# Optimization experiments

Hardware: AMD Instinct MI355X
Metric: run time of the kernel (lower is better)

The kernel has to match this reference:

```python
import jax, jax.numpy as jnp
import numpy as np

WORD_TOTAL = 1_000_000
POS_TOTAL = 123
DIM = 50        # word embedding dim
DWPE = 5        # position embedding dim
C = 230         # conv filters (dimensionC)
WIN = 3         # conv window
REL = 53        # relationTotal
B = 1024        # bag size (number of sentences)
L = 128         # sentence length


def setup_inputs() -> dict:
    key = jax.random.key(0)
    ks = jax.random.split(key, 12)
    con = np.sqrt(6.0 / (C + REL))
    con1 = np.sqrt(6.0 / ((DWPE + DIM) * WIN))
    inp = {
        "sen": jax.random.randint(ks[0], (B, L), 0, WORD_TOTAL),
        "p1": jax.random.randint(ks[1], (B, L), 0, POS_TOTAL),
        "p2": jax.random.randint(ks[2], (B, L), 0, POS_TOTAL),
        "wordVec": jax.random.normal(ks[3], (WORD_TOTAL, DIM), jnp.float32) * 0.05,
        "posVec1": jax.random.normal(ks[4], (POS_TOTAL, DWPE), jnp.float32) * con1,
        "posVec2": jax.random.normal(ks[5], (POS_TOTAL, DWPE), jnp.float32) * con1,
        "Wv": jax.random.normal(ks[6], (WIN, DIM, C), jnp.float32) * 0.05,
        "Wp1": jax.random.normal(ks[7], (WIN, DWPE, C), jnp.float32) * 0.05,
        "Wp2": jax.random.normal(ks[8], (WIN, DWPE, C), jnp.float32) * 0.05,
        "bv": jnp.zeros((C,), jnp.float32),
        "bp1": jnp.zeros((C,), jnp.float32),
        "bp2": jnp.zeros((C,), jnp.float32),
        "attW": jax.random.normal(ks[9], (C, C), jnp.float32) * con,
        "MR": jax.random.normal(ks[10], (C, REL), jnp.float32) * 0.05,
        "MRb": jnp.zeros((REL,), jnp.float32),
        "rel": 7,
    }
    return inp


def _conv_full_width(emb, W):
    Lout = emb.shape[1] - WIN + 1
    wins = jnp.stack([emb[:, j:j + Lout, :] for j in range(WIN)], axis=0)
    return jnp.einsum('jbld,jdc->blc', wins, W)  # [B, Lout, C]


def reference(sen, p1, p2, wordVec, posVec1, posVec2, Wv, bv, Wp1, bp1, Wp2, bp2, attW, MR, MRb, rel):
    # ---- encode: per-sentence PCNN-style encoder, batched over the bag ----
    ev = wordVec[sen]   # [B, L, DIM]
    e1 = posVec1[p1]    # [B, L, DWPE]
    e2 = posVec2[p2]    # [B, L, DWPE]
    c = (_conv_full_width(ev, Wv) + bv
         + _conv_full_width(e1, Wp1) + bp1
         + _conv_full_width(e2, Wp2) + bp2)          # [B, Lout, C]
    cnn_output = jnp.tanh(jnp.max(c, axis=1))          # [B, C]
    # ---- selective attention over the bag (training=False: dropout identity) ----
    scores = (cnn_output @ attW) @ MR + MRb            # [B, REL]
    weight = jax.nn.softmax(scores[:, rel])            # [B] = exp/sum(exp)
    att_output = jnp.sum(weight[:, None] * cnn_output, axis=0)[None, :]  # [1, C]
    output = jax.nn.softmax(att_output @ MR + MRb)     # [1, REL]
    return (output, att_output, cnn_output, weight[:, None])
```

## Files before the change

kernel.cpp:

```cpp
#include <hip/hip_runtime.h>
#include <math.h>

#define CCH 230
#define REL 53
#define BAG 1024
#define SLEN 128
#define LOUT 126

typedef __bf16 bf16x8 __attribute__((ext_vector_type(8)));
typedef float f32x4 __attribute__((ext_vector_type(4)));

#define WS_BF_USHORTS (16 * 6 * 64 * 8)
#define WS_BSUM 24576
#define WS_V    24832
#define WS_SCORES 25088

__device__ __forceinline__ unsigned short f2bf(float f) {
    unsigned u = __builtin_bit_cast(unsigned, f);
    unsigned r = (u + 0x7fffu + ((u >> 16) & 1u)) >> 16;
    return (unsigned short)r;
}

__global__ void pa_kernel(const float* __restrict__ Wv, const float* __restrict__ Wp1,
                          const float* __restrict__ Wp2, const float* __restrict__ bv,
                          const float* __restrict__ bp1, const float* __restrict__ bp2,
                          const float* __restrict__ attW, const float* __restrict__ MR,
                          const int* __restrict__ relp, float* __restrict__ ws) {
    if (blockIdx.x < 193) {
        int idx = blockIdx.x * 256 + threadIdx.x;
        if (idx < WS_BF_USHORTS) {
            int j = idx & 7;
            int lane = (idx >> 3) & 63;
            int q = idx >> 9;
            int ks = q % 6, ntile = q / 6;
            int n = ntile * 16 + (lane & 15);
            int k = ks * 32 + (lane >> 4) * 8 + j;
            float v = 0.f;
            if (k < 180 && n < CCH) {
                int jw = k / 60;
                int d = k - jw * 60;
                if (d < 50)      v = Wv[(jw * 50 + d) * CCH + n];
                else if (d < 55) v = Wp1[(jw * 5 + (d - 50)) * CCH + n];
                else             v = Wp2[(jw * 5 + (d - 55)) * CCH + n];
            }
            ((unsigned short*)ws)[idx] = f2bf(v);
        } else {
            int ch = idx - WS_BF_USHORTS;
            float v = 0.f;
            if (ch < CCH) v = bv[ch] + bp1[ch] + bp2[ch];
            ws[WS_BSUM + ch] = v;
        }
    } else {
        int i = (blockIdx.x - 193) * 4 + (threadIdx.x >> 6);
        int lane = threadIdx.x & 63;
        if (i < CCH) {
            int rel = *relp;
            float s = 0.f;
            for (int j = lane; j < CCH; j += 64) s += attW[i * CCH + j] * MR[j * REL + rel];
            for (int off = 32; off > 0; off >>= 1) s += __shfl_down(s, off, 64);
            if (lane == 0) ws[WS_V + i] = s;
        }
    }
}

__global__ __launch_bounds__(512, 4) void conv_kernel(
    const int* __restrict__ sen, const int* __restrict__ p1, const int* __restrict__ p2,
    const float* __restrict__ wordVec, const float* __restrict__ posVec1,
    const float* __restrict__ posVec2, const float* __restrict__ ws,
    const float* __restrict__ MRb, const int* __restrict__ relp,
    float* __restrict__ cnn_out, float* __restrict__ scores) {
    __shared__ __align__(16) unsigned short x_lds[132 * 60];
    __shared__ int s_idx[3][SLEN];
    __shared__ float s_red[8];
    const int b = blockIdx.x;
    const int tid = threadIdx.x;
    const int lane = tid & 63, w = tid >> 6;
    const int quad = lane >> 4, l16 = lane & 15;
    const unsigned short* wsu = (const unsigned short*)ws;

    bf16x8 bfrag[6][2];
    #pragma unroll
    for (int ks = 0; ks < 6; ++ks)
        #pragma unroll
        for (int nt = 0; nt < 2; ++nt) {
            int ntile = w * 2 + nt;
            bfrag[ks][nt] = *reinterpret_cast<const bf16x8*>(wsu + ((ntile * 6 + ks) * 64 + lane) * 8);
        }

    if (tid < 384) {
        int a = tid >> 7, i = tid & 127;
        const int* src = (a == 0) ? sen : (a == 1) ? p1 : p2;
        s_idx[a][i] = src[b * SLEN + i];
    }
    __syncthreads();

    {
        int l = tid >> 2, t = tid & 3;
        if (t < 3) {
            float v[16];
            const float* base = wordVec + s_idx[0][l] * 50 + t * 16;
            #pragma unroll
            for (int k2 = 0; k2 < 8; ++k2) {
                float2 f = *reinterpret_cast<const float2*>(base + 2 * k2);
                v[2 * k2] = f.x; v[2 * k2 + 1] = f.y;
            }
            ushort4* dst = reinterpret_cast<ushort4*>(x_lds + l * 60 + t * 16);
            #pragma unroll
            for (int q = 0; q < 4; ++q) {
                ushort4 o;
                o.x = f2bf(v[4 * q + 0]); o.y = f2bf(v[4 * q + 1]);
                o.z = f2bf(v[4 * q + 2]); o.w = f2bf(v[4 * q + 3]);
                dst[q] = o;
            }
        } else {
            float v[12];
            float2 wv = *reinterpret_cast<const float2*>(wordVec + s_idx[0][l] * 50 + 48);
            v[0] = wv.x; v[1] = wv.y;
            int i1 = s_idx[1][l] * 5, i2 = s_idx[2][l] * 5;
            #pragma unroll
            for (int j = 0; j < 5; ++j) { v[2 + j] = posVec1[i1 + j]; v[7 + j] = posVec2[i2 + j]; }
            ushort4* dst = reinterpret_cast<ushort4*>(x_lds + l * 60 + 48);
            #pragma unroll
            for (int q = 0; q < 3; ++q) {
                ushort4 o;
                o.x = f2bf(v[4 * q + 0]); o.y = f2bf(v[4 * q + 1]);
                o.z = f2bf(v[4 * q + 2]); o.w = f2bf(v[4 * q + 3]);
                dst[q] = o;
            }
        }
    }
    if (tid < 16) {
        int l = SLEN + (tid >> 2), t = tid & 3;
        ushort4 z; z.x = z.y = z.z = z.w = 0;
        ushort4* dst = reinterpret_cast<ushort4*>(x_lds + l * 60 + ((t < 3) ? t * 16 : 48));
        if (t < 3) { dst[0] = z; dst[1] = z; dst[2] = z; dst[3] = z; }
        else       { dst[0] = z; dst[1] = z; dst[2] = z; }
    }
    __syncthreads();

    f32x4 acc[8][2];
    #pragma unroll
    for (int mt = 0; mt < 8; ++mt)
        #pragma unroll
        for (int nt = 0; nt < 2; ++nt) acc[mt][nt] = (f32x4){0.f, 0.f, 0.f, 0.f};

    union AU { uint2 u2[2]; bf16x8 v; };

    #pragma unroll
    for (int ks = 0; ks < 6; ++ks) {
        int kg = ks * 4 + quad;
        #pragma unroll
        for (int mt = 0; mt < 8; ++mt) {
            int m = mt * 16 + l16;
            const uint2* ap = reinterpret_cast<const uint2*>(x_lds + m * 60 + kg * 8);
            AU a; a.u2[0] = ap[0]; a.u2[1] = ap[1];
            #pragma unroll
            for (int nt = 0; nt < 2; ++nt)
                acc[mt][nt] = __builtin_amdgcn_mfma_f32_16x16x32_bf16(a.v, bfrag[ks][nt], acc[mt][nt], 0, 0, 0);
        }
    }

    float vals[2];
    #pragma unroll
    for (int nt = 0; nt < 2; ++nt) {
        float mv = -3.0e38f;
        #pragma unroll
        for (int mt = 0; mt < 8; ++mt) {
            #pragma unroll
            for (int r = 0; r < 4; ++r) {
                int l = mt * 16 + quad * 4 + r;
                if (l < LOUT) mv = fmaxf(mv, acc[mt][nt][r]);
            }
        }
        mv = fmaxf(mv, __shfl_xor(mv, 16, 64));
        mv = fmaxf(mv, __shfl_xor(mv, 32, 64));
        int ch = w * 32 + nt * 16 + l16;
        float t = tanhf(mv + ws[WS_BSUM + ch]);
        vals[nt] = t;
        if (quad == 0 && ch < CCH) cnn_out[b * CCH + ch] = t;
    }

    float s = 0.f;
    if (quad == 0) {
        #pragma unroll
        for (int nt = 0; nt < 2; ++nt) {
            int ch = w * 32 + nt * 16 + l16;
            if (ch < CCH) s += vals[nt] * ws[WS_V + ch];
        }
    }
    for (int off = 32; off > 0; off >>= 1) s += __shfl_down(s, off, 64);
    if (lane == 0) s_red[w] = s;
    __syncthreads();
    if (tid == 0) {
        float t = MRb[*relp];
        #pragma unroll
        for (int i = 0; i < 8; ++i) t += s_red[i];
        scores[b] = t;
    }
}

__global__ void final_kernel(const float* __restrict__ cnn, const float* __restrict__ MR,
                             const float* __restrict__ MRb, const float* __restrict__ scores,
                             float* __restrict__ out0, float* __restrict__ att_out,
                             float* __restrict__ w_out) {
    __shared__ float red[1024];
    __shared__ float wbuf[1024];
    __shared__ float abuf[256];
    __shared__ float lbuf[64];
    __shared__ float MRs[CCH * REL];
    int tid = threadIdx.x;

    for (int i = tid; i < CCH * REL; i += 1024) MRs[i] = MR[i];

    float s = scores[tid];
    red[tid] = s; __syncthreads();
    for (int off = 512; off > 0; off >>= 1) {
        if (tid < off) red[tid] = fmaxf(red[tid], red[tid + off]);
        __syncthreads();
    }
    float mx = red[0]; __syncthreads();
    float e = expf(s - mx);
    red[tid] = e; __syncthreads();
    for (int off = 512; off > 0; off >>= 1) {
        if (tid < off) red[tid] += red[tid + off];
        __syncthreads();
    }
    float sum = red[0]; __syncthreads();
    float w = e / sum;
    w_out[tid] = w;
    wbuf[tid] = w;
    __syncthreads();

    int ch = tid & 255, grp = tid >> 8;
    float a = 0.f;
    if (ch < CCH) {
        int bb0 = grp * 256;
        #pragma unroll 16
        for (int bb = bb0; bb < bb0 + 256; ++bb) a += wbuf[bb] * cnn[bb * CCH + ch];
    }
    red[grp * 256 + ch] = a;
    __syncthreads();
    float t = 0.f;
    if (tid < 256) {
        float att = red[tid] + red[256 + tid] + red[512 + tid] + red[768 + tid];
        if (tid < CCH) { att_out[tid] = att; abuf[tid] = att; }
    }
    __syncthreads();
    if (tid < REL) {
        t = MRb[tid];
        #pragma unroll 10
        for (int c = 0; c < CCH; ++c) t += abuf[c] * MRs[c * REL + tid];
        lbuf[tid] = t;
    }
    __syncthreads();
    if (tid == 0) {
        float m2 = -3.0e38f;
        for (int i = 0; i < REL; ++i) m2 = fmaxf(m2, lbuf[i]);
        float s2 = 0.f;
        for (int i = 0; i < REL; ++i) s2 += expf(lbuf[i] - m2);
        lbuf[60] = m2; lbuf[61] = s2;
    }
    __syncthreads();
    if (tid < REL) out0[tid] = expf(t - lbuf[60]) / lbuf[61];
}

extern "C" void kernel_launch(void* const* d_in, const int* in_sizes, int n_in,
                              void* d_out, int out_size, void* d_ws, size_t ws_size,
                              hipStream_t stream) {
    const int* sen = (const int*)d_in[0];
    const int* p1  = (const int*)d_in[1];
    const int* p2  = (const int*)d_in[2];
    const float* wordVec = (const float*)d_in[3];
    const float* posVec1 = (const float*)d_in[4];
    const float* posVec2 = (const float*)d_in[5];
    const float* Wv  = (const float*)d_in[6];
    const float* Wp1 = (const float*)d_in[7];
    const float* Wp2 = (const float*)d_in[8];
    const float* bv  = (const float*)d_in[9];
    const float* bp1 = (const float*)d_in[10];
    const float* bp2 = (const float*)d_in[11];
    const float* attW = (const float*)d_in[12];
    const float* MR  = (const float*)d_in[13];
    const float* MRb = (const float*)d_in[14];
    const int* relp  = (const int*)d_in[15];

    float* ws = (float*)d_ws;
    float* out = (float*)d_out;
    float* out0    = out;
    float* att_out = out + REL;
    float* cnn_out = out + REL + CCH;
    float* w_out   = out + REL + CCH + BAG * CCH;

    hipLaunchKernelGGL(pa_kernel, dim3(193 + 58), dim3(256), 0, stream,
                       Wv, Wp1, Wp2, bv, bp1, bp2, attW, MR, relp, ws);
    hipLaunchKernelGGL(conv_kernel, dim3(BAG), dim3(512), 0, stream,
                       sen, p1, p2, wordVec, posVec1, posVec2, ws, MRb, relp,
                       cnn_out, ws + WS_SCORES);
    hipLaunchKernelGGL(final_kernel, dim3(1), dim3(1024), 0, stream,
                       cnn_out, MR, MRb, ws + WS_SCORES, out0, att_out, w_out);
}
```

Before: 313.9 us.

## Split bag-attention reduction across blocks with atomics and drop index staging

The single-block final kernel is replaced by a 32-block kernel. Each block recomputes the softmax over scores, builds weights for its own 32 sentences and atomically adds its partial weighted sum into att_out, which pa_kernel now zeroes first. A small second kernel then computes the relation logits and softmax. Separately, the conv kernel reads the sentence and position indices straight from global memory instead of staging them in LDS behind a barrier. This adds one kernel launch and makes the att_out sum order nondeterministic because of the float atomics.

```diff
diff --git a/kernel.cpp b/kernel.cpp
--- a/kernel.cpp
+++ b/kernel.cpp
@@ -25,7 +25,8 @@
                           const float* __restrict__ Wp2, const float* __restrict__ bv,
                           const float* __restrict__ bp1, const float* __restrict__ bp2,
                           const float* __restrict__ attW, const float* __restrict__ MR,
-                          const int* __restrict__ relp, float* __restrict__ ws) {
+                          const int* __restrict__ relp, float* __restrict__ ws,
+                          float* __restrict__ att_out) {
     if (blockIdx.x < 193) {
         int idx = blockIdx.x * 256 + threadIdx.x;
         if (idx < WS_BF_USHORTS) {
@@ -47,7 +48,7 @@
         } else {
             int ch = idx - WS_BF_USHORTS;
             float v = 0.f;
-            if (ch < CCH) v = bv[ch] + bp1[ch] + bp2[ch];
+            if (ch < CCH) { v = bv[ch] + bp1[ch] + bp2[ch]; att_out[ch] = 0.f; }
             ws[WS_BSUM + ch] = v;
         }
     } else {
@@ -70,7 +71,6 @@
     const float* __restrict__ MRb, const int* __restrict__ relp,
     float* __restrict__ cnn_out, float* __restrict__ scores) {
     __shared__ __align__(16) unsigned short x_lds[132 * 60];
-    __shared__ int s_idx[3][SLEN];
     __shared__ float s_red[8];
     const int b = blockIdx.x;
     const int tid = threadIdx.x;
@@ -87,18 +87,12 @@
             bfrag[ks][nt] = *reinterpret_cast<const bf16x8*>(wsu + ((ntile * 6 + ks) * 64 + lane) * 8);
         }
 
-    if (tid < 384) {
-        int a = tid >> 7, i = tid & 127;
-        const int* src = (a == 0) ? sen : (a == 1) ? p1 : p2;
-        s_idx[a][i] = src[b * SLEN + i];
-    }
-    __syncthreads();
-
     {
         int l = tid >> 2, t = tid & 3;
+        int si = sen[b * SLEN + l];
         if (t < 3) {
             float v[16];
-            const float* base = wordVec + s_idx[0][l] * 50 + t * 16;
+            const float* base = wordVec + si * 50 + t * 16;
             #pragma unroll
             for (int k2 = 0; k2 < 8; ++k2) {
                 float2 f = *reinterpret_cast<const float2*>(base + 2 * k2);
@@ -114,9 +108,9 @@
             }
         } else {
             float v[12];
-            float2 wv = *reinterpret_cast<const float2*>(wordVec + s_idx[0][l] * 50 + 48);
+            float2 wv = *reinterpret_cast<const float2*>(wordVec + si * 50 + 48);
             v[0] = wv.x; v[1] = wv.y;
-            int i1 = s_idx[1][l] * 5, i2 = s_idx[2][l] * 5;
+            int i1 = p1[b * SLEN + l] * 5, i2 = p2[b * SLEN + l] * 5;
             #pragma unroll
             for (int j = 0; j < 5; ++j) { v[2 + j] = posVec1[i1 + j]; v[7 + j] = posVec2[i2 + j]; }
             ushort4* dst = reinterpret_cast<ushort4*>(x_lds + l * 60 + 48);
@@ -199,57 +193,58 @@
     }
 }
 
-__global__ void final_kernel(const float* __restrict__ cnn, const float* __restrict__ MR,
-                             const float* __restrict__ MRb, const float* __restrict__ scores,
-                             float* __restrict__ out0, float* __restrict__ att_out,
-                             float* __restrict__ w_out) {
-    __shared__ float red[1024];
-    __shared__ float wbuf[1024];
-    __shared__ float abuf[256];
+__global__ void final1_kernel(const float* __restrict__ cnn, const float* __restrict__ scores,
+                              float* __restrict__ att_out, float* __restrict__ w_out) {
+    __shared__ float redm[4], reds[4];
+    __shared__ float wloc[32];
+    int tid = threadIdx.x, g = blockIdx.x;
+    float s0[4];
+    float mx = -3.0e38f;
+    #pragma unroll
+    for (int k = 0; k < 4; ++k) { s0[k] = scores[tid + 256 * k]; mx = fmaxf(mx, s0[k]); }
+    #pragma unroll
+    for (int off = 32; off > 0; off >>= 1) mx = fmaxf(mx, __shfl_xor(mx, off, 64));
+    if ((tid & 63) == 0) redm[tid >> 6] = mx;
+    __syncthreads();
+    mx = fmaxf(fmaxf(redm[0], redm[1]), fmaxf(redm[2], redm[3]));
+    float sum = 0.f;
+    #pragma unroll
+    for (int k = 0; k < 4; ++k) sum += expf(s0[k] - mx);
+    #pragma unroll
+    for (int off = 32; off > 0; off >>= 1) sum += __shfl_xor(sum, off, 64);
+    if ((tid & 63) == 0) reds[tid >> 6] = sum;
+    __syncthreads();
+    sum = reds[0] + reds[1] + reds[2] + reds[3];
+
+    int b0 = g * 32;
+    if (tid < 32) {
+        float w = expf(scores[b0 + tid] - mx) / sum;
+        wloc[tid] = w;
+        w_out[b0 + tid] = w;
+    }
+    __syncthreads();
+    if (tid < CCH) {
+        float a = 0.f;
+        #pragma unroll 8
+        for (int bb = 0; bb < 32; ++bb) a += wloc[bb] * cnn[(b0 + bb) * CCH + tid];
+        atomicAdd(&att_out[tid], a);
+    }
+}
+
+__global__ void final2_kernel(const float* __restrict__ att_in, const float* __restrict__ MR,
+                              const float* __restrict__ MRb, float* __restrict__ out0) {
+    __shared__ float MRs[CCH * REL];
+    __shared__ float atts[CCH];
     __shared__ float lbuf[64];
-    __shared__ float MRs[CCH * REL];
     int tid = threadIdx.x;
-
-    for (int i = tid; i < CCH * REL; i += 1024) MRs[i] = MR[i];
-
-    float s = scores[tid];
-    red[tid] = s; __syncthreads();
-    for (int off = 512; off > 0; off >>= 1) {
-        if (tid < off) red[tid] = fmaxf(red[tid], red[tid + off]);
-        __syncthreads();
-    }
-    float mx = red[0]; __syncthreads();
-    float e = expf(s - mx);
-    red[tid] = e; __syncthreads();
-    for (int off = 512; off > 0; off >>= 1) {
-        if (tid < off) red[tid] += red[tid + off];
-        __syncthreads();
-    }
-    float sum = red[0]; __syncthreads();
-    float w = e / sum;
-    w_out[tid] = w;
-    wbuf[tid] = w;
-    __syncthreads();
-
-    int ch = tid & 255, grp = tid >> 8;
-    float a = 0.f;
-    if (ch < CCH) {
-        int bb0 = grp * 256;
-        #pragma unroll 16
-        for (int bb = bb0; bb < bb0 + 256; ++bb) a += wbuf[bb] * cnn[bb * CCH + ch];
-    }
-    red[grp * 256 + ch] = a;
+    for (int i = tid; i < CCH * REL; i += 256) MRs[i] = MR[i];
+    if (tid < CCH) atts[tid] = att_in[tid];
     __syncthreads();
     float t = 0.f;
-    if (tid < 256) {
-        float att = red[tid] + red[256 + tid] + red[512 + tid] + red[768 + tid];
-        if (tid < CCH) { att_out[tid] = att; abuf[tid] = att; }
-    }
-    __syncthreads();
     if (tid < REL) {
         t = MRb[tid];
         #pragma unroll 10
-        for (int c = 0; c < CCH; ++c) t += abuf[c] * MRs[c * REL + tid];
+        for (int c = 0; c < CCH; ++c) t += atts[c] * MRs[c * REL + tid];
         lbuf[tid] = t;
     }
     __syncthreads();
@@ -292,10 +287,12 @@
     float* w_out   = out + REL + CCH + BAG * CCH;
 
     hipLaunchKernelGGL(pa_kernel, dim3(193 + 58), dim3(256), 0, stream,
-                       Wv, Wp1, Wp2, bv, bp1, bp2, attW, MR, relp, ws);
+                       Wv, Wp1, Wp2, bv, bp1, bp2, attW, MR, relp, ws, att_out);
     hipLaunchKernelGGL(conv_kernel, dim3(BAG), dim3(512), 0, stream,
                        sen, p1, p2, wordVec, posVec1, posVec2, ws, MRb, relp,
                        cnn_out, ws + WS_SCORES);
-    hipLaunchKernelGGL(final_kernel, dim3(1), dim3(1024), 0, stream,
-                       cnn_out, MR, MRb, ws + WS_SCORES, out0, att_out, w_out);
-}
+    hipLaunchKernelGGL(final1_kernel, dim3(32), dim3(256), 0, stream,
+                       cnn_out, ws + WS_SCORES, att_out, w_out);
+    hipLaunchKernelGGL(final2_kernel, dim3(1), dim3(256), 0, stream,
+                       att_out, MR, MRb, out0);
+}
```

After: 303.4 us. -3.3%, faster.
